# Optimization experiments

Measured on AMD Instinct MI355X. Metric: run time of the kernel, lower is better.

The kernel has to match this reference:

```python
import jax, jax.numpy as jnp
import numpy as np

N_NODES = 50000


def _gcn_conv(x, W, b, src, dst, n_nodes):
    """PyG GCNConv: add self-loops, symmetric normalization, aggregate, linear, bias.
    x: [N, Fin], W: [Fin, Fout], b: [Fout], src/dst: [E] int.
    """
    loop = jnp.arange(n_nodes, dtype=src.dtype)
    src_f = jnp.concatenate([src, loop])  # [E + N]
    dst_f = jnp.concatenate([dst, loop])
    # degree over incoming edges (edge weights are all 1 after self-loops)
    deg = jax.ops.segment_sum(jnp.ones_like(src_f, dtype=x.dtype), dst_f,
                              num_segments=n_nodes)
    dinv = jnp.where(deg > 0, jax.lax.rsqrt(deg), 0.0)
    norm = dinv[src_f] * dinv[dst_f]  # [E + N]
    h = x @ W  # [N, Fout] -- transform before propagate (Fin >= Fout path)
    msg = h[src_f] * norm[:, None]  # gather + per-edge scale
    out = jax.ops.segment_sum(msg, dst_f, num_segments=n_nodes)  # scatter-add
    return out + b


def setup_inputs() -> dict:
    key = jax.random.key(0)
    k_x, k_e, k_w1, k_w2 = jax.random.split(key, 4)
    in_ch, out_ch = 128, 64
    hid = 2 * out_ch
    n_edges = 800000
    x = jax.random.normal(k_x, (N_NODES, in_ch), dtype=jnp.float32)
    edge_index = jax.random.randint(k_e, (2, n_edges), 0, N_NODES, dtype=jnp.int64)
    # Glorot-ish init for weights, zero bias (matches PyG defaults)
    W1 = jax.random.normal(k_w1, (in_ch, hid), dtype=jnp.float32) / np.sqrt(in_ch)
    b1 = jnp.zeros((hid,), dtype=jnp.float32)
    W2 = jax.random.normal(k_w2, (hid, out_ch), dtype=jnp.float32) / np.sqrt(hid)
    b2 = jnp.zeros((out_ch,), dtype=jnp.float32)
    return {"x": x, "edge_index": edge_index, "W1": W1, "b1": b1, "W2": W2, "b2": b2}


def reference(x, edge_index, W1, b1, W2, b2):
    src, dst = edge_index[0], edge_index[1]
    h = jnp.tanh(_gcn_conv(x, W1, b1, src, dst, N_NODES))
    return _gcn_conv(h, W2, b2, src, dst, N_NODES)
```

## Files before the change

### kernel.cpp

```cpp
#include <hip/hip_runtime.h>
#include <stdint.h>

#define N_NODES 50000
#define IN_CH   128
#define HID     128
#define OUT_CH  64

#define CBITS 8
#define NCB   196
#define CAP   8192
#define APB   4096

#define XPAD  136
#define G1BLK 782

typedef unsigned int   uint32;
typedef unsigned short ushort16;
typedef __attribute__((ext_vector_type(8))) short short8;
typedef __attribute__((ext_vector_type(4))) float f32x4;

static __device__ __forceinline__ ushort16 f32_to_bf16(float f) {
    uint32 u = __float_as_uint(f);
    u = (u + 0x7fffu + ((u >> 16) & 1u)) >> 16;
    return (ushort16)u;
}
static __device__ __forceinline__ float bf16lo_to_f32(uint32 u) {
    return __uint_as_float(u << 16);
}
static __device__ __forceinline__ float bf16hi_to_f32(uint32 u) {
    return __uint_as_float(u & 0xffff0000u);
}
#define RLI(v, l) __builtin_amdgcn_readlane((v), (l))
#define RLF(v, l) __uint_as_float((uint32)__builtin_amdgcn_readlane((int)__float_as_uint(v), (l)))

__global__ __launch_bounds__(256) void prep_kernel(
    const float* __restrict__ W1, const float* __restrict__ W2,
    ushort16* __restrict__ w1t, ushort16* __restrict__ w2t,
    int* __restrict__ gcur) {
    const int t = threadIdx.x;
    if (blockIdx.x == 64) {
        if (t < NCB) gcur[t] = 0;
        return;
    }
    int i = blockIdx.x * 256 + t;
    if (i < 128 * 128) {
        int k = i >> 7, n = i & 127;
        w1t[n * 128 + k] = f32_to_bf16(W1[k * 128 + n]);
    }
    if (i < 128 * 64) {
        int k = i >> 6, n = i & 63;
        w2t[n * 128 + k] = f32_to_bf16(W2[k * 64 + n]);
    }
}

__global__ __launch_bounds__(256) void build1_kernel(
    const int* __restrict__ src, const int* __restrict__ dst,
    int* __restrict__ gcur, uint32* __restrict__ ebuf2, int E, int nA,
    const float* __restrict__ x, const ushort16* __restrict__ w1t,
    ushort16* __restrict__ h1b) {
    __shared__ __align__(16) char smem[52224];
    const int t = threadIdx.x;

    if ((int)blockIdx.x >= nA) {
        ushort16* xs = (ushort16*)smem;
        ushort16* wt = (ushort16*)(smem + 64 * XPAD * 2);
        const int block_row = ((int)blockIdx.x - nA) * 64;

        {
            const uint4* g = (const uint4*)w1t;
            #pragma unroll
            for (int j = 0; j < 8; ++j) {
                int idx = t + 256 * j;
                int row = idx >> 4, c = idx & 15;
                uint4 v = g[idx];
                *(uint4*)&wt[row * XPAD + c * 8] = v;
            }
        }
        {
            #pragma unroll
            for (int j = 0; j < 8; ++j) {
                int idx = t + 256 * j;
                int row = idx >> 5, c4 = idx & 31;
                int gr = block_row + row; if (gr >= N_NODES) gr = N_NODES - 1;
                float4 v = *(const float4*)(x + (size_t)gr * IN_CH + c4 * 4);
                uint32 p0 = (uint32)f32_to_bf16(v.x) | ((uint32)f32_to_bf16(v.y) << 16);
                uint32 p1 = (uint32)f32_to_bf16(v.z) | ((uint32)f32_to_bf16(v.w) << 16);
                uint32* dp = (uint32*)&xs[row * XPAD + c4 * 4];
                dp[0] = p0; dp[1] = p1;
            }
        }
        __syncthreads();

        const int wv = t >> 6, lane = t & 63;
        const int r16 = lane & 15, kq = lane >> 4;
        f32x4 acc[8];
        #pragma unroll
        for (int n = 0; n < 8; ++n) acc[n] = (f32x4){0.f, 0.f, 0.f, 0.f};

        const ushort16* xrow = &xs[(wv * 16 + r16) * XPAD + kq * 8];
        #pragma unroll
        for (int kk = 0; kk < 4; ++kk) {
            short8 a = *(const short8*)(xrow + kk * 32);
            #pragma unroll
            for (int n = 0; n < 8; ++n) {
                short8 b = *(const short8*)&wt[(n * 16 + r16) * XPAD + kk * 32 + kq * 8];
                acc[n] = __builtin_amdgcn_mfma_f32_16x16x32_bf16(a, b, acc[n], 0, 0, 0);
            }
        }

        #pragma unroll
        for (int n = 0; n < 8; ++n) {
            #pragma unroll
            for (int j = 0; j < 4; ++j) {
                int gr = block_row + wv * 16 + kq * 4 + j;
                if (gr < N_NODES)
                    h1b[(size_t)gr * HID + n * 16 + r16] = f32_to_bf16(acc[n][j]);
            }
        }
        return;
    }

    int* hist = (int*)smem;
    int* excl = hist + 256;
    int* fcur = excl + 256;
    int* gbase = fcur + 256;
    uint32* obuf = (uint32*)(gbase + 256);

    const int e0 = blockIdx.x * APB;
    const int nv = min(APB, E - e0);

    hist[t] = 0;
    __syncthreads();

    uint32 u[16];
    #pragma unroll
    for (int j = 0; j < 16; ++j) {
        int i = t + 256 * j;
        u[j] = 0xffffffffu;
        if (i < nv) {
            int e = e0 + i;
            int s = src[e], d = dst[e];
            if ((unsigned)d < N_NODES && (unsigned)s < N_NODES) {
                u[j] = (uint32)s | ((uint32)d << 16);
                atomicAdd(&hist[(unsigned)d >> CBITS], 1);
            }
        }
    }
    __syncthreads();

    excl[t] = hist[t];
    __syncthreads();
    #pragma unroll
    for (int off = 1; off < 256; off <<= 1) {
        int v = (t >= off) ? excl[t - off] : 0;
        __syncthreads();
        excl[t] += v;
        __syncthreads();
    }
    int myexcl = excl[t] - hist[t];
    int gb = 0;
    if (hist[t] > 0) gb = t * CAP + atomicAdd(&gcur[t], hist[t]);
    __syncthreads();
    excl[t] = myexcl;
    fcur[t] = myexcl;
    gbase[t] = gb;
    __syncthreads();

    #pragma unroll
    for (int j = 0; j < 16; ++j) {
        if (u[j] != 0xffffffffu) {
            int b = u[j] >> (16 + CBITS);
            int pos = atomicAdd(&fcur[b], 1);
            obuf[pos] = u[j];
        }
    }
    __syncthreads();

    for (int i = t; i < nv; i += 256) {
        uint32 v = obuf[i];
        int b = v >> (16 + CBITS);
        int gpos = gbase[b] + (i - excl[b]);
        if (gpos < (b + 1) * CAP) ebuf2[gpos] = v;
    }
}

__global__ __launch_bounds__(256) void build2_kernel(
    const uint32* __restrict__ ebuf2, const int* __restrict__ gcur,
    ushort16* __restrict__ ebuf16, int* __restrict__ offs,
    int* __restrict__ degi, float* __restrict__ dinv) {
    __shared__ __align__(16) char smem[53248];
    uint32*   sbuf = (uint32*)smem;
    ushort16* obuf = (ushort16*)(smem + CAP * 4);
    int* fh = (int*)(smem + CAP * 4 + CAP * 2);
    int* fx = fh + 256;
    int* fc = fx + 256;
    int* gs = fc + 256;
    const int b = blockIdx.x, t = threadIdx.x;

    {
        int c = (t < NCB) ? min(gcur[t], CAP) : 0;
        gs[t] = c;
        __syncthreads();
        #pragma unroll
        for (int off = 1; off < 256; off <<= 1) {
            int v = (t >= off) ? gs[t - off] : 0;
            __syncthreads();
            gs[t] += v;
            __syncthreads();
        }
    }
    const int nb = min(gcur[b], CAP);
    const int obase = gs[b] - nb;
    __syncthreads();

    fh[t] = 0;
    __syncthreads();
    for (int i = t; i < nb; i += 256) {
        uint32 v = ebuf2[b * CAP + i];
        sbuf[i] = v;
        atomicAdd(&fh[(v >> 16) & 255], 1);
    }
    __syncthreads();

    fx[t] = fh[t];
    __syncthreads();
    #pragma unroll
    for (int off = 1; off < 256; off <<= 1) {
        int v = (t >= off) ? fx[t - off] : 0;
        __syncthreads();
        fx[t] += v;
        __syncthreads();
    }
    int ex = fx[t] - fh[t];
    fc[t] = ex;

    int n = b * 256 + t;
    if (n < N_NODES) {
        degi[n] = fh[t];
        offs[n] = obase + ex;
        dinv[n] = rsqrtf(1.0f + (float)fh[t]);
    }
    __syncthreads();

    for (int i = t; i < nb; i += 256) {
        uint32 v = sbuf[i];
        int nl = (v >> 16) & 255;
        int pos = atomicAdd(&fc[nl], 1);
        obuf[pos] = (ushort16)(v & 0xffffu);
    }
    __syncthreads();
    for (int i = t; i < nb; i += 256) ebuf16[obase + i] = obuf[i];
}

__global__ __launch_bounds__(256) void gather1_kernel(
    const int* __restrict__ offs, const int* __restrict__ degi,
    const ushort16* __restrict__ ebuf16, const float* __restrict__ dinv,
    const ushort16* __restrict__ h1b, const float* __restrict__ b1,
    ushort16* __restrict__ a1b) {
    int node = blockIdx.x * 4 + (threadIdx.x >> 6);
    int lane = threadIdx.x & 63;
    if (node >= N_NODES) return;
    float di = dinv[node];
    int beg = offs[node];
    int cnt = degi[node];

    uint32 us = ((const uint32*)(h1b + (size_t)node * HID))[lane];
    float ax = bf16lo_to_f32(us) * di * di;
    float ay = bf16hi_to_f32(us) * di * di;

    for (int base = 0; base < cnt; base += 64) {
        int m = min(cnt - base, 64);
        int e_l = 0; float w_l = 0.f;
        if (lane < m) {
            e_l = (int)ebuf16[beg + base + lane];
            e_l = min(e_l, N_NODES - 1);
            w_l = dinv[e_l] * di;
        }
        int i = 0;
        for (; i + 8 <= m; i += 8) {
            int s0 = RLI(e_l, i),     s1 = RLI(e_l, i + 1);
            int s2 = RLI(e_l, i + 2), s3 = RLI(e_l, i + 3);
            int s4 = RLI(e_l, i + 4), s5 = RLI(e_l, i + 5);
            int s6 = RLI(e_l, i + 6), s7 = RLI(e_l, i + 7);
            float w0 = RLF(w_l, i),     w1 = RLF(w_l, i + 1);
            float w2 = RLF(w_l, i + 2), w3 = RLF(w_l, i + 3);
            float w4 = RLF(w_l, i + 4), w5 = RLF(w_l, i + 5);
            float w6 = RLF(w_l, i + 6), w7 = RLF(w_l, i + 7);
            uint32 u0 = ((const uint32*)(h1b + (size_t)s0 * HID))[lane];
            uint32 u1 = ((const uint32*)(h1b + (size_t)s1 * HID))[lane];
            uint32 u2 = ((const uint32*)(h1b + (size_t)s2 * HID))[lane];
            uint32 u3 = ((const uint32*)(h1b + (size_t)s3 * HID))[lane];
            uint32 u4 = ((const uint32*)(h1b + (size_t)s4 * HID))[lane];
            uint32 u5 = ((const uint32*)(h1b + (size_t)s5 * HID))[lane];
            uint32 u6 = ((const uint32*)(h1b + (size_t)s6 * HID))[lane];
            uint32 u7 = ((const uint32*)(h1b + (size_t)s7 * HID))[lane];
            ax += bf16lo_to_f32(u0) * w0 + bf16lo_to_f32(u1) * w1
                + bf16lo_to_f32(u2) * w2 + bf16lo_to_f32(u3) * w3
                + bf16lo_to_f32(u4) * w4 + bf16lo_to_f32(u5) * w5
                + bf16lo_to_f32(u6) * w6 + bf16lo_to_f32(u7) * w7;
            ay += bf16hi_to_f32(u0) * w0 + bf16hi_to_f32(u1) * w1
                + bf16hi_to_f32(u2) * w2 + bf16hi_to_f32(u3) * w3
                + bf16hi_to_f32(u4) * w4 + bf16hi_to_f32(u5) * w5
                + bf16hi_to_f32(u6) * w6 + bf16hi_to_f32(u7) * w7;
        }
        if (i + 4 <= m) {
            int s0 = RLI(e_l, i),     s1 = RLI(e_l, i + 1);
            int s2 = RLI(e_l, i + 2), s3 = RLI(e_l, i + 3);
            float w0 = RLF(w_l, i),     w1 = RLF(w_l, i + 1);
            float w2 = RLF(w_l, i + 2), w3 = RLF(w_l, i + 3);
            uint32 u0 = ((const uint32*)(h1b + (size_t)s0 * HID))[lane];
            uint32 u1 = ((const uint32*)(h1b + (size_t)s1 * HID))[lane];
            uint32 u2 = ((const uint32*)(h1b + (size_t)s2 * HID))[lane];
            uint32 u3 = ((const uint32*)(h1b + (size_t)s3 * HID))[lane];
            ax += bf16lo_to_f32(u0) * w0 + bf16lo_to_f32(u1) * w1
                + bf16lo_to_f32(u2) * w2 + bf16lo_to_f32(u3) * w3;
            ay += bf16hi_to_f32(u0) * w0 + bf16hi_to_f32(u1) * w1
                + bf16hi_to_f32(u2) * w2 + bf16hi_to_f32(u3) * w3;
            i += 4;
        }
        for (; i < m; ++i) {
            int s0 = RLI(e_l, i);
            float w0 = RLF(w_l, i);
            uint32 u0 = ((const uint32*)(h1b + (size_t)s0 * HID))[lane];
            ax += bf16lo_to_f32(u0) * w0;
            ay += bf16hi_to_f32(u0) * w0;
        }
    }
    float2 bb = ((const float2*)b1)[lane];
    float tx = tanhf(ax + bb.x);
    float ty = tanhf(ay + bb.y);
    uint32 pk = (uint32)f32_to_bf16(tx) | ((uint32)f32_to_bf16(ty) << 16);
    ((uint32*)(a1b + (size_t)node * HID))[lane] = pk;
}

__global__ __launch_bounds__(256) void gemm2_mfma_kernel(
    const ushort16* __restrict__ a1b, const ushort16* __restrict__ w2t,
    const float* __restrict__ dinv, ushort16* __restrict__ h2s) {
    __shared__ __align__(16) ushort16 xs[64 * XPAD];
    __shared__ __align__(16) ushort16 wt[64 * XPAD];
    const int tid = threadIdx.x;
    const int block_row = blockIdx.x * 64;

    {
        const uint4* g = (const uint4*)w2t;
        #pragma unroll
        for (int j = 0; j < 4; ++j) {
            int idx = tid + 256 * j;
            int row = idx >> 4, c = idx & 15;
            uint4 v = g[idx];
            *(uint4*)&wt[row * XPAD + c * 8] = v;
        }
    }
    {
        #pragma unroll
        for (int j = 0; j < 4; ++j) {
            int idx = tid + 256 * j;
            int row = idx >> 4, c = idx & 15;
            int gr = block_row + row; if (gr >= N_NODES) gr = N_NODES - 1;
            uint4 v = *(const uint4*)(a1b + (size_t)gr * HID + c * 8);
            *(uint4*)&xs[row * XPAD + c * 8] = v;
        }
    }
    __syncthreads();

    const int wv = tid >> 6, lane = tid & 63;
    const int r16 = lane & 15, kq = lane >> 4;
    f32x4 acc[4];
    #pragma unroll
    for (int n = 0; n < 4; ++n) acc[n] = (f32x4){0.f, 0.f, 0.f, 0.f};

    const ushort16* xrow = &xs[(wv * 16 + r16) * XPAD + kq * 8];
    #pragma unroll
    for (int kk = 0; kk < 4; ++kk) {
        short8 a = *(const short8*)(xrow + kk * 32);
        #pragma unroll
        for (int n = 0; n < 4; ++n) {
            short8 b = *(const short8*)&wt[(n * 16 + r16) * XPAD + kk * 32 + kq * 8];
            acc[n] = __builtin_amdgcn_mfma_f32_16x16x32_bf16(a, b, acc[n], 0, 0, 0);
        }
    }

    #pragma unroll
    for (int j = 0; j < 4; ++j) {
        int gr = block_row + wv * 16 + kq * 4 + j;
        if (gr < N_NODES) {
            float dv = dinv[gr];
            #pragma unroll
            for (int n = 0; n < 4; ++n)
                h2s[(size_t)gr * OUT_CH + n * 16 + r16] = f32_to_bf16(acc[n][j] * dv);
        }
    }
}

__global__ __launch_bounds__(256) void gather2_kernel(
    const int* __restrict__ offs, const int* __restrict__ degi,
    const ushort16* __restrict__ ebuf16, const float* __restrict__ dinv,
    const ushort16* __restrict__ h2s, const float* __restrict__ b2,
    float* __restrict__ out) {
    int node = blockIdx.x * 4 + (threadIdx.x >> 6);
    int lane = threadIdx.x & 63;
    if (node >= N_NODES) return;
    float di = dinv[node];
    int beg = offs[node];
    int cnt = degi[node];

    float acc = __uint_as_float(((uint32)h2s[(size_t)node * OUT_CH + lane]) << 16);

    for (int base = 0; base < cnt; base += 64) {
        int m = min(cnt - base, 64);
        int e_l = 0;
        if (lane < m) {
            e_l = (int)ebuf16[beg + base + lane];
            e_l = min(e_l, N_NODES - 1);
        }
        int i = 0;
        for (; i + 8 <= m; i += 8) {
            int s0 = RLI(e_l, i),     s1 = RLI(e_l, i + 1);
            int s2 = RLI(e_l, i + 2), s3 = RLI(e_l, i + 3);
            int s4 = RLI(e_l, i + 4), s5 = RLI(e_l, i + 5);
            int s6 = RLI(e_l, i + 6), s7 = RLI(e_l, i + 7);
            float v0 = __uint_as_float(((uint32)h2s[(size_t)s0 * OUT_CH + lane]) << 16);
            float v1 = __uint_as_float(((uint32)h2s[(size_t)s1 * OUT_CH + lane]) << 16);
            float v2 = __uint_as_float(((uint32)h2s[(size_t)s2 * OUT_CH + lane]) << 16);
            float v3 = __uint_as_float(((uint32)h2s[(size_t)s3 * OUT_CH + lane]) << 16);
            float v4 = __uint_as_float(((uint32)h2s[(size_t)s4 * OUT_CH + lane]) << 16);
            float v5 = __uint_as_float(((uint32)h2s[(size_t)s5 * OUT_CH + lane]) << 16);
            float v6 = __uint_as_float(((uint32)h2s[(size_t)s6 * OUT_CH + lane]) << 16);
            float v7 = __uint_as_float(((uint32)h2s[(size_t)s7 * OUT_CH + lane]) << 16);
            acc += ((v0 + v1) + (v2 + v3)) + ((v4 + v5) + (v6 + v7));
        }
        if (i + 4 <= m) {
            int s0 = RLI(e_l, i),     s1 = RLI(e_l, i + 1);
            int s2 = RLI(e_l, i + 2), s3 = RLI(e_l, i + 3);
            float v0 = __uint_as_float(((uint32)h2s[(size_t)s0 * OUT_CH + lane]) << 16);
            float v1 = __uint_as_float(((uint32)h2s[(size_t)s1 * OUT_CH + lane]) << 16);
            float v2 = __uint_as_float(((uint32)h2s[(size_t)s2 * OUT_CH + lane]) << 16);
            float v3 = __uint_as_float(((uint32)h2s[(size_t)s3 * OUT_CH + lane]) << 16);
            acc += (v0 + v1) + (v2 + v3);
            i += 4;
        }
        for (; i < m; ++i) {
            int s0 = RLI(e_l, i);
            acc += __uint_as_float(((uint32)h2s[(size_t)s0 * OUT_CH + lane]) << 16);
        }
    }
    out[(size_t)node * OUT_CH + lane] = b2[lane] + di * acc;
}

extern "C" void kernel_launch(void* const* d_in, const int* in_sizes, int n_in,
                              void* d_out, int out_size, void* d_ws, size_t ws_size,
                              hipStream_t stream) {
    const float* x  = (const float*)d_in[0];
    const int*   ei = (const int*)d_in[1];
    const float* W1 = (const float*)d_in[2];
    const float* b1 = (const float*)d_in[3];
    const float* W2 = (const float*)d_in[4];
    const float* b2 = (const float*)d_in[5];
    float* out = (float*)d_out;

    const int E = in_sizes[1] / 2;
    const int* src = ei;
    const int* dst = ei + E;
    const int nA = (E + APB - 1) / APB;

    float* dinv   = (float*)d_ws;
    int* degi     = (int*)(dinv + N_NODES);
    int* offs     = degi + N_NODES;
    int* gcur     = offs + N_NODES;
    ushort16* w1t = (ushort16*)(gcur + NCB);
    ushort16* w2t = w1t + 128 * 128;
    ushort16* ebuf16 = w2t + 64 * 128;
    uintptr_t p   = (uintptr_t)(ebuf16 + (size_t)NCB * CAP);
    p = (p + 15) & ~(uintptr_t)15;
    ushort16* a1b = (ushort16*)p;
    uint32* ebuf2 = (uint32*)a1b;
    ushort16* h1b = a1b + (size_t)N_NODES * HID;
    ushort16* h2s = h1b + (size_t)N_NODES * HID;

    prep_kernel<<<65, 256, 0, stream>>>(W1, W2, w1t, w2t, gcur);
    build1_kernel<<<nA + G1BLK, 256, 0, stream>>>(src, dst, gcur, ebuf2, E, nA,
                                                  x, w1t, h1b);
    build2_kernel<<<NCB, 256, 0, stream>>>(ebuf2, gcur, ebuf16, offs, degi, dinv);
    gather1_kernel<<<(N_NODES + 3) / 4, 256, 0, stream>>>(offs, degi, ebuf16, dinv, h1b, b1, a1b);
    gemm2_mfma_kernel<<<G1BLK, 256, 0, stream>>>(a1b, w2t, dinv, h2s);
    gather2_kernel<<<(N_NODES + 3) / 4, 256, 0, stream>>>(offs, degi, ebuf16, dinv, h2s, b2, out);
}
```

Before: 108.2 us.

## Prescale layer-1 features by source dinv and compute degrees via global atomics

Layer-1 GEMM now runs inside build2 and scales each row of h1 by rsqrt(1+deg) before storing, so gather1 sums rows without per-edge weights and applies the destination dinv once at the end. Degrees are now counted with global atomics from extra build1 blocks, after zeroing in prep, so they are ready before the GEMM. This removes per-edge dinv gathers and readlanes in gather1. In exchange it adds 800K global atomics, and the GEMM is moved out of overlap with the bucketing phase.

```diff
diff --git a/kernel.cpp b/kernel.cpp
--- a/kernel.cpp
+++ b/kernel.cpp
@@ -31,18 +31,23 @@
     return __uint_as_float(u & 0xffff0000u);
 }
 #define RLI(v, l) __builtin_amdgcn_readlane((v), (l))
-#define RLF(v, l) __uint_as_float((uint32)__builtin_amdgcn_readlane((int)__float_as_uint(v), (l)))
 
 __global__ __launch_bounds__(256) void prep_kernel(
     const float* __restrict__ W1, const float* __restrict__ W2,
     ushort16* __restrict__ w1t, ushort16* __restrict__ w2t,
-    int* __restrict__ gcur) {
+    int* __restrict__ gcur, int* __restrict__ degi) {
     const int t = threadIdx.x;
-    if (blockIdx.x == 64) {
+    const int b = blockIdx.x;
+    if (b == 64) {
         if (t < NCB) gcur[t] = 0;
         return;
     }
-    int i = blockIdx.x * 256 + t;
+    if (b >= 65) {
+        int i = (b - 65) * 256 + t;
+        if (i < N_NODES) degi[i] = 0;
+        return;
+    }
+    int i = b * 256 + t;
     if (i < 128 * 128) {
         int k = i >> 7, n = i & 127;
         w1t[n * 128 + k] = f32_to_bf16(W1[k * 128 + n]);
@@ -56,15 +61,101 @@
 __global__ __launch_bounds__(256) void build1_kernel(
     const int* __restrict__ src, const int* __restrict__ dst,
     int* __restrict__ gcur, uint32* __restrict__ ebuf2, int E, int nA,
+    int* __restrict__ degi) {
+    __shared__ __align__(16) char smem[20992];
+    const int t = threadIdx.x;
+
+    if ((int)blockIdx.x >= nA) {
+        const int e0 = ((int)blockIdx.x - nA) * APB;
+        #pragma unroll
+        for (int j = 0; j < 16; ++j) {
+            int i = e0 + t + 256 * j;
+            if (i < E) {
+                int s = src[i], d = dst[i];
+                if ((unsigned)d < N_NODES && (unsigned)s < N_NODES)
+                    atomicAdd(&degi[d], 1);
+            }
+        }
+        return;
+    }
+
+    int* hist = (int*)smem;
+    int* excl = hist + 256;
+    int* fcur = excl + 256;
+    int* gbase = fcur + 256;
+    uint32* obuf = (uint32*)(gbase + 256);
+
+    const int e0 = blockIdx.x * APB;
+    const int nv = min(APB, E - e0);
+
+    hist[t] = 0;
+    __syncthreads();
+
+    uint32 u[16];
+    #pragma unroll
+    for (int j = 0; j < 16; ++j) {
+        int i = t + 256 * j;
+        u[j] = 0xffffffffu;
+        if (i < nv) {
+            int e = e0 + i;
+            int s = src[e], d = dst[e];
+            if ((unsigned)d < N_NODES && (unsigned)s < N_NODES) {
+                u[j] = (uint32)s | ((uint32)d << 16);
+                atomicAdd(&hist[(unsigned)d >> CBITS], 1);
+            }
+        }
+    }
+    __syncthreads();
+
+    excl[t] = hist[t];
+    __syncthreads();
+    #pragma unroll
+    for (int off = 1; off < 256; off <<= 1) {
+        int v = (t >= off) ? excl[t - off] : 0;
+        __syncthreads();
+        excl[t] += v;
+        __syncthreads();
+    }
+    int myexcl = excl[t] - hist[t];
+    int gb = 0;
+    if (hist[t] > 0) gb = t * CAP + atomicAdd(&gcur[t], hist[t]);
+    __syncthreads();
+    excl[t] = myexcl;
+    fcur[t] = myexcl;
+    gbase[t] = gb;
+    __syncthreads();
+
+    #pragma unroll
+    for (int j = 0; j < 16; ++j) {
+        if (u[j] != 0xffffffffu) {
+            int b = u[j] >> (16 + CBITS);
+            int pos = atomicAdd(&fcur[b], 1);
+            obuf[pos] = u[j];
+        }
+    }
+    __syncthreads();
+
+    for (int i = t; i < nv; i += 256) {
+        uint32 v = obuf[i];
+        int b = v >> (16 + CBITS);
+        int gpos = gbase[b] + (i - excl[b]);
+        if (gpos < (b + 1) * CAP) ebuf2[gpos] = v;
+    }
+}
+
+__global__ __launch_bounds__(256) void build2_kernel(
+    const uint32* __restrict__ ebuf2, const int* __restrict__ gcur,
+    ushort16* __restrict__ ebuf16, int* __restrict__ offs,
+    const int* __restrict__ degi, float* __restrict__ dinv,
     const float* __restrict__ x, const ushort16* __restrict__ w1t,
-    ushort16* __restrict__ h1b) {
-    __shared__ __align__(16) char smem[52224];
+    ushort16* __restrict__ h1s) {
+    __shared__ __align__(16) char smem[53248];
     const int t = threadIdx.x;
 
-    if ((int)blockIdx.x >= nA) {
+    if ((int)blockIdx.x >= NCB) {
         ushort16* xs = (ushort16*)smem;
         ushort16* wt = (ushort16*)(smem + 64 * XPAD * 2);
-        const int block_row = ((int)blockIdx.x - nA) * 64;
+        const int block_row = ((int)blockIdx.x - NCB) * 64;
 
         {
             const uint4* g = (const uint4*)w1t;
@@ -109,93 +200,25 @@
         }
 
         #pragma unroll
-        for (int n = 0; n < 8; ++n) {
-            #pragma unroll
-            for (int j = 0; j < 4; ++j) {
-                int gr = block_row + wv * 16 + kq * 4 + j;
-                if (gr < N_NODES)
-                    h1b[(size_t)gr * HID + n * 16 + r16] = f32_to_bf16(acc[n][j]);
+        for (int j = 0; j < 4; ++j) {
+            int gr = block_row + wv * 16 + kq * 4 + j;
+            if (gr < N_NODES) {
+                float dv = rsqrtf(1.0f + (float)degi[gr]);
+                #pragma unroll
+                for (int n = 0; n < 8; ++n)
+                    h1s[(size_t)gr * HID + n * 16 + r16] = f32_to_bf16(acc[n][j] * dv);
             }
         }
         return;
     }
 
-    int* hist = (int*)smem;
-    int* excl = hist + 256;
-    int* fcur = excl + 256;
-    int* gbase = fcur + 256;
-    uint32* obuf = (uint32*)(gbase + 256);
-
-    const int e0 = blockIdx.x * APB;
-    const int nv = min(APB, E - e0);
-
-    hist[t] = 0;
-    __syncthreads();
-
-    uint32 u[16];
-    #pragma unroll
-    for (int j = 0; j < 16; ++j) {
-        int i = t + 256 * j;
-        u[j] = 0xffffffffu;
-        if (i < nv) {
-            int e = e0 + i;
-            int s = src[e], d = dst[e];
-            if ((unsigned)d < N_NODES && (unsigned)s < N_NODES) {
-                u[j] = (uint32)s | ((uint32)d << 16);
-                atomicAdd(&hist[(unsigned)d >> CBITS], 1);
-            }
-        }
-    }
-    __syncthreads();
-
-    excl[t] = hist[t];
-    __syncthreads();
-    #pragma unroll
-    for (int off = 1; off < 256; off <<= 1) {
-        int v = (t >= off) ? excl[t - off] : 0;
-        __syncthreads();
-        excl[t] += v;
-        __syncthreads();
-    }
-    int myexcl = excl[t] - hist[t];
-    int gb = 0;
-    if (hist[t] > 0) gb = t * CAP + atomicAdd(&gcur[t], hist[t]);
-    __syncthreads();
-    excl[t] = myexcl;
-    fcur[t] = myexcl;
-    gbase[t] = gb;
-    __syncthreads();
-
-    #pragma unroll
-    for (int j = 0; j < 16; ++j) {
-        if (u[j] != 0xffffffffu) {
-            int b = u[j] >> (16 + CBITS);
-            int pos = atomicAdd(&fcur[b], 1);
-            obuf[pos] = u[j];
-        }
-    }
-    __syncthreads();
-
-    for (int i = t; i < nv; i += 256) {
-        uint32 v = obuf[i];
-        int b = v >> (16 + CBITS);
-        int gpos = gbase[b] + (i - excl[b]);
-        if (gpos < (b + 1) * CAP) ebuf2[gpos] = v;
-    }
-}
-
-__global__ __launch_bounds__(256) void build2_kernel(
-    const uint32* __restrict__ ebuf2, const int* __restrict__ gcur,
-    ushort16* __restrict__ ebuf16, int* __restrict__ offs,
-    int* __restrict__ degi, float* __restrict__ dinv) {
-    __shared__ __align__(16) char smem[53248];
     uint32*   sbuf = (uint32*)smem;
     ushort16* obuf = (ushort16*)(smem + CAP * 4);
     int* fh = (int*)(smem + CAP * 4 + CAP * 2);
     int* fx = fh + 256;
     int* fc = fx + 256;
     int* gs = fc + 256;
-    const int b = blockIdx.x, t = threadIdx.x;
+    const int b = blockIdx.x;
 
     {
         int c = (t < NCB) ? min(gcur[t], CAP) : 0;
@@ -236,7 +259,6 @@
 
     int n = b * 256 + t;
     if (n < N_NODES) {
-        degi[n] = fh[t];
         offs[n] = obase + ex;
         dinv[n] = rsqrtf(1.0f + (float)fh[t]);
     }
@@ -255,7 +277,7 @@
 __global__ __launch_bounds__(256) void gather1_kernel(
     const int* __restrict__ offs, const int* __restrict__ degi,
     const ushort16* __restrict__ ebuf16, const float* __restrict__ dinv,
-    const ushort16* __restrict__ h1b, const float* __restrict__ b1,
+    const ushort16* __restrict__ h1s, const float* __restrict__ b1,
     ushort16* __restrict__ a1b) {
     int node = blockIdx.x * 4 + (threadIdx.x >> 6);
     int lane = threadIdx.x & 63;
@@ -264,17 +286,16 @@
     int beg = offs[node];
     int cnt = degi[node];
 
-    uint32 us = ((const uint32*)(h1b + (size_t)node * HID))[lane];
-    float ax = bf16lo_to_f32(us) * di * di;
-    float ay = bf16hi_to_f32(us) * di * di;
+    uint32 us = ((const uint32*)(h1s + (size_t)node * HID))[lane];
+    float ax = bf16lo_to_f32(us);
+    float ay = bf16hi_to_f32(us);
 
     for (int base = 0; base < cnt; base += 64) {
         int m = min(cnt - base, 64);
-        int e_l = 0; float w_l = 0.f;
+        int e_l = 0;
         if (lane < m) {
             e_l = (int)ebuf16[beg + base + lane];
             e_l = min(e_l, N_NODES - 1);
-            w_l = dinv[e_l] * di;
         }
         int i = 0;
         for (; i + 8 <= m; i += 8) {
@@ -282,53 +303,46 @@
             int s2 = RLI(e_l, i + 2), s3 = RLI(e_l, i + 3);
             int s4 = RLI(e_l, i + 4), s5 = RLI(e_l, i + 5);
             int s6 = RLI(e_l, i + 6), s7 = RLI(e_l, i + 7);
-            float w0 = RLF(w_l, i),     w1 = RLF(w_l, i + 1);
-            float w2 = RLF(w_l, i + 2), w3 = RLF(w_l, i + 3);
-            float w4 = RLF(w_l, i + 4), w5 = RLF(w_l, i + 5);
-            float w6 = RLF(w_l, i + 6), w7 = RLF(w_l, i + 7);
-            uint32 u0 = ((const uint32*)(h1b + (size_t)s0 * HID))[lane];
-            uint32 u1 = ((const uint32*)(h1b + (size_t)s1 * HID))[lane];
-            uint32 u2 = ((const uint32*)(h1b + (size_t)s2 * HID))[lane];
-            uint32 u3 = ((const uint32*)(h1b + (size_t)s3 * HID))[lane];
-            uint32 u4 = ((const uint32*)(h1b + (size_t)s4 * HID))[lane];
-            uint32 u5 = ((const uint32*)(h1b + (size_t)s5 * HID))[lane];
-            uint32 u6 = ((const uint32*)(h1b + (size_t)s6 * HID))[lane];
-            uint32 u7 = ((const uint32*)(h1b + (size_t)s7 * HID))[lane];
-            ax += bf16lo_to_f32(u0) * w0 + bf16lo_to_f32(u1) * w1
-                + bf16lo_to_f32(u2) * w2 + bf16lo_to_f32(u3) * w3
-                + bf16lo_to_f32(u4) * w4 + bf16lo_to_f32(u5) * w5
-                + bf16lo_to_f32(u6) * w6 + bf16lo_to_f32(u7) * w7;
-            ay += bf16hi_to_f32(u0) * w0 + bf16hi_to_f32(u1) * w1
-                + bf16hi_to_f32(u2) * w2 + bf16hi_to_f32(u3) * w3
-                + bf16hi_to_f32(u4) * w4 + bf16hi_to_f32(u5) * w5
-                + bf16hi_to_f32(u6) * w6 + bf16hi_to_f32(u7) * w7;
+            uint32 u0 = ((const uint32*)(h1s + (size_t)s0 * HID))[lane];
+            uint32 u1 = ((const uint32*)(h1s + (size_t)s1 * HID))[lane];
+            uint32 u2 = ((const uint32*)(h1s + (size_t)s2 * HID))[lane];
+            uint32 u3 = ((const uint32*)(h1s + (size_t)s3 * HID))[lane];
+            uint32 u4 = ((const uint32*)(h1s + (size_t)s4 * HID))[lane];
+            uint32 u5 = ((const uint32*)(h1s + (size_t)s5 * HID))[lane];
+            uint32 u6 = ((const uint32*)(h1s + (size_t)s6 * HID))[lane];
+            uint32 u7 = ((const uint32*)(h1s + (size_t)s7 * HID))[lane];
+            ax += (bf16lo_to_f32(u0) + bf16lo_to_f32(u1))
+                + (bf16lo_to_f32(u2) + bf16lo_to_f32(u3))
+                + (bf16lo_to_f32(u4) + bf16lo_to_f32(u5))
+                + (bf16lo_to_f32(u6) + bf16lo_to_f32(u7));
+            ay += (bf16hi_to_f32(u0) + bf16hi_to_f32(u1))
+                + (bf16hi_to_f32(u2) + bf16hi_to_f32(u3))
+                + (bf16hi_to_f32(u4) + bf16hi_to_f32(u5))
+                + (bf16hi_to_f32(u6) + bf16hi_to_f32(u7));
         }
         if (i + 4 <= m) {
             int s0 = RLI(e_l, i),     s1 = RLI(e_l, i + 1);
             int s2 = RLI(e_l, i + 2), s3 = RLI(e_l, i + 3);
-            float w0 = RLF(w_l, i),     w1 = RLF(w_l, i + 1);
-            float w2 = RLF(w_l, i + 2), w3 = RLF(w_l, i + 3);
-            uint32 u0 = ((const uint32*)(h1b + (size_t)s0 * HID))[lane];
-            uint32 u1 = ((const uint32*)(h1b + (size_t)s1 * HID))[lane];
-            uint32 u2 = ((const uint32*)(h1b + (size_t)s2 * HID))[lane];
-            uint32 u3 = ((const uint32*)(h1b + (size_t)s3 * HID))[lane];
-            ax += bf16lo_to_f32(u0) * w0 + bf16lo_to_f32(u1) * w1
-                + bf16lo_to_f32(u2) * w2 + bf16lo_to_f32(u3) * w3;
-            ay += bf16hi_to_f32(u0) * w0 + bf16hi_to_f32(u1) * w1
-                + bf16hi_to_f32(u2) * w2 + bf16hi_to_f32(u3) * w3;
+            uint32 u0 = ((const uint32*)(h1s + (size_t)s0 * HID))[lane];
+            uint32 u1 = ((const uint32*)(h1s + (size_t)s1 * HID))[lane];
+            uint32 u2 = ((const uint32*)(h1s + (size_t)s2 * HID))[lane];
+            uint32 u3 = ((const uint32*)(h1s + (size_t)s3 * HID))[lane];
+            ax += (bf16lo_to_f32(u0) + bf16lo_to_f32(u1))
+                + (bf16lo_to_f32(u2) + bf16lo_to_f32(u3));
+            ay += (bf16hi_to_f32(u0) + bf16hi_to_f32(u1))
+                + (bf16hi_to_f32(u2) + bf16hi_to_f32(u3));
             i += 4;
         }
         for (; i < m; ++i) {
             int s0 = RLI(e_l, i);
-            float w0 = RLF(w_l, i);
-            uint32 u0 = ((const uint32*)(h1b + (size_t)s0 * HID))[lane];
-            ax += bf16lo_to_f32(u0) * w0;
-            ay += bf16hi_to_f32(u0) * w0;
+            uint32 u0 = ((const uint32*)(h1s + (size_t)s0 * HID))[lane];
+            ax += bf16lo_to_f32(u0);
+            ay += bf16hi_to_f32(u0);
         }
     }
     float2 bb = ((const float2*)b1)[lane];
-    float tx = tanhf(ax + bb.x);
-    float ty = tanhf(ay + bb.y);
+    float tx = tanhf(di * ax + bb.x);
+    float ty = tanhf(di * ay + bb.y);
     uint32 pk = (uint32)f32_to_bf16(tx) | ((uint32)f32_to_bf16(ty) << 16);
     ((uint32*)(a1b + (size_t)node * HID))[lane] = pk;
 }
@@ -462,6 +476,7 @@
     const int* src = ei;
     const int* dst = ei + E;
     const int nA = (E + APB - 1) / APB;
+    const int nD = (E + APB - 1) / APB;
 
     float* dinv   = (float*)d_ws;
     int* degi     = (int*)(dinv + N_NODES);
@@ -474,14 +489,14 @@
     p = (p + 15) & ~(uintptr_t)15;
     ushort16* a1b = (ushort16*)p;
     uint32* ebuf2 = (uint32*)a1b;
-    ushort16* h1b = a1b + (size_t)N_NODES * HID;
-    ushort16* h2s = h1b + (size_t)N_NODES * HID;
-
-    prep_kernel<<<65, 256, 0, stream>>>(W1, W2, w1t, w2t, gcur);
-    build1_kernel<<<nA + G1BLK, 256, 0, stream>>>(src, dst, gcur, ebuf2, E, nA,
-                                                  x, w1t, h1b);
-    build2_kernel<<<NCB, 256, 0, stream>>>(ebuf2, gcur, ebuf16, offs, degi, dinv);
-    gather1_kernel<<<(N_NODES + 3) / 4, 256, 0, stream>>>(offs, degi, ebuf16, dinv, h1b, b1, a1b);
+    ushort16* h1s = a1b + (size_t)N_NODES * HID;
+    ushort16* h2s = h1s + (size_t)N_NODES * HID;
+
+    prep_kernel<<<65 + (N_NODES + 255) / 256, 256, 0, stream>>>(W1, W2, w1t, w2t, gcur, degi);
+    build1_kernel<<<nA + nD, 256, 0, stream>>>(src, dst, gcur, ebuf2, E, nA, degi);
+    build2_kernel<<<NCB + G1BLK, 256, 0, stream>>>(ebuf2, gcur, ebuf16, offs, degi, dinv,
+                                                   x, w1t, h1s);
+    gather1_kernel<<<(N_NODES + 3) / 4, 256, 0, stream>>>(offs, degi, ebuf16, dinv, h1s, b1, a1b);
     gemm2_mfma_kernel<<<G1BLK, 256, 0, stream>>>(a1b, w2t, dinv, h2s);
     gather2_kernel<<<(N_NODES + 3) / 4, 256, 0, stream>>>(offs, degi, ebuf16, dinv, h2s, b2, out);
 }
```

Result: slower. 133.0 us (+22.8%).
